# Kernel optimization log

Hardware: AMD Instinct MI355X
Metric: run time of the kernel (lower is better)

## Reference

```python
import jax, jax.numpy as jnp
import numpy as np

H, I, B, S = 3200, 12800, 8, 1024  # InternViT-6B MLP dims


def setup_inputs() -> dict:
    key = jax.random.key(0)
    ks = jax.random.split(key, 8)
    # int8-valued activations/weights stored as int32 (harness dtype set)
    hidden_states = jax.random.randint(ks[0], (B, S, H), -127, 128, dtype=jnp.int32)
    scale = jax.random.uniform(ks[1], (B * S,), dtype=jnp.float32) * 1e-3 + 1e-5
    w1 = jax.random.randint(ks[2], (I, H), -127, 128, dtype=jnp.int32)
    w1_scale = jax.random.uniform(ks[3], (I,), dtype=jnp.float32) * 1e-3 + 1e-5
    b1 = jax.random.normal(ks[4], (I,), dtype=jnp.float32) * 0.02
    w2 = jax.random.randint(ks[5], (H, I), -127, 128, dtype=jnp.int32)
    w2_scale = jax.random.uniform(ks[6], (H,), dtype=jnp.float32) * 1e-3 + 1e-5
    b2 = jax.random.normal(ks[7], (H,), dtype=jnp.float32) * 0.02
    return {"hidden_states": hidden_states, "scale": scale, "w1": w1,
            "w1_scale": w1_scale, "b1": b1, "w2": w2, "w2_scale": w2_scale, "b2": b2}


def _w8a8_linear(x_q, x_scale, w_q, w_scale, b):
    # enough that fp32 matmul reproduces the exact integer accumulator to
    # within float32 rounding of the final sum.
    acc = jnp.matmul(x_q.astype(jnp.float32), w_q.astype(jnp.float32).T)  # [T, out]
    out = acc * x_scale[:, None] * w_scale[None, :] + b[None, :]
    return out.astype(jnp.float16)


def reference(hidden_states, scale, w1, w1_scale, b1, w2, w2_scale, b2):
    bsz, seq, hidden = hidden_states.shape
    x_q = hidden_states.reshape(-1, hidden)                 # [T, H] int8 values
    # fc1: W8A8 -> fp16 with dynamic per-token input scale
    fc1_out = _w8a8_linear(x_q, scale, w1, w1_scale, b1)    # [T, I] fp16
    # fused gelu_and_quant: exact GELU, then per-token dynamic int8 re-quant
    g = jax.nn.gelu(fc1_out.astype(jnp.float32), approximate=False)  # [T, I]
    new_scale = jnp.max(jnp.abs(g), axis=-1) / 127.0        # dynamic per-token scale
    act_q = jnp.clip(jnp.round(g / new_scale[:, None]), -127, 127)  # int8 values
    # fc2: W8A8 -> fp16
    out = _w8a8_linear(act_q, new_scale, w2, w2_scale, b2)  # [T, H] fp16
    return out
```

## Files before the change

### kernel.cpp

```cpp
#include <hip/hip_runtime.h>
#include <hip/hip_bf16.h>
#include <hip/hip_fp16.h>

#define T_DIM 8192
#define H_DIM 3200
#define I_DIM 12800

typedef int v4i __attribute__((ext_vector_type(4)));
typedef _Float16 h8 __attribute__((ext_vector_type(8)));

__device__ __forceinline__ void gload16(const void* g, void* l) {
    __builtin_amdgcn_global_load_lds(
        (const __attribute__((address_space(1))) unsigned int*)g,
        (__attribute__((address_space(3))) unsigned int*)l, 16, 0, 0);
}

__global__ __launch_bounds__(256) void repack_kernel(const int* __restrict__ src,
                                                     unsigned int* __restrict__ dst,
                                                     long n4) {
    long i = (long)blockIdx.x * blockDim.x + threadIdx.x;
    long stride = (long)gridDim.x * blockDim.x;
    for (; i < n4; i += stride) {
        int4 v = ((const int4*)src)[i];
        dst[i] = (unsigned int)((v.x & 255) | ((v.y & 255) << 8) |
                                ((v.z & 255) << 16) | ((v.w & 255) << 24));
    }
}

template <int EPI>
__global__ __launch_bounds__(512, 2) void gemm_i8_8ph(
    const signed char* __restrict__ A, long strideA,
    const signed char* __restrict__ B, long strideB,
    int Ntrue, int K, int ldc,
    const float* __restrict__ rowscale, const float* __restrict__ colscale,
    const float* __restrict__ bias, void* __restrict__ Cout) {
    __shared__ signed char lds[131072];
    signed char* ldsA = lds;
    signed char* ldsB = lds + 65536;

    const int tid = threadIdx.x;
    const int lane = tid & 63, wid = tid >> 6;
    const int wr = wid >> 2, wc = wid & 3;
    const int bm = blockIdx.x, bn = blockIdx.y;
    const long Arow0 = (long)bm * 256;
    const long Bcol0 = (long)bn * 256;

    const int c0 = tid, c1 = tid + 512;
    const int r0 = c0 >> 2, r1 = c1 >> 2;
    const int s0 = (((c0 & 3) ^ ((r0 >> 1) & 3)) << 4);
    const int s1 = (((c1 & 3) ^ ((r1 >> 1) & 3)) << 4);
    const signed char* Ag0 = A + (Arow0 + r0) * strideA + s0;
    const signed char* Ag1 = A + (Arow0 + r1) * strideA + s1;
    const signed char* Bg0 = B + (Bcol0 + r0) * strideB + s0;
    const signed char* Bg1 = B + (Bcol0 + r1) * strideB + s1;
    const int d0 = c0 * 16, d1 = c1 * 16;

    const int NH = K >> 6;
    const int nkt = K >> 7;

#define STAGE_A(h)                                  \
    {                                               \
        const int hc_ = (h) < NH ? (h) : NH - 1;    \
        const long ko_ = (long)hc_ << 6;            \
        signed char* d_ = ldsA + (((h) & 3) << 14); \
        gload16(Ag0 + ko_, d_ + d0);                \
        gload16(Ag1 + ko_, d_ + d1);                \
    }
#define STAGE_B(h)                                  \
    {                                               \
        const int hc_ = (h) < NH ? (h) : NH - 1;    \
        const long ko_ = (long)hc_ << 6;            \
        signed char* d_ = ldsB + (((h) & 3) << 14); \
        gload16(Bg0 + ko_, d_ + d0);                \
        gload16(Bg1 + ko_, d_ + d1);                \
    }

    const int r = lane & 15, q = lane >> 4;
    const int swz = ((q ^ ((r >> 1) & 3)) << 4);
    const int aoff = (wr * 128 + r) * 64 + swz;
    const int boff = (wc * 64 + r) * 64 + swz;

    v4i acc[8][4] = {};
    v4i af[4], bf[4];

#define PHASE(SLOTA, SLOTB, AIDX, LOADB, ACCOFF, STAGE_STMT, GATE_STMT)     \
    {                                                                       \
        _Pragma("unroll") for (int i = 0; i < 4; ++i)                       \
            af[i] = *(const v4i*)((SLOTA) + aoff + ((AIDX) + i) * 1024);    \
        if (LOADB) {                                                        \
            _Pragma("unroll") for (int n = 0; n < 4; ++n)                   \
                bf[n] = *(const v4i*)((SLOTB) + boff + n * 1024);           \
        }                                                                   \
        STAGE_STMT;                                                         \
        __builtin_amdgcn_s_barrier();                                       \
        asm volatile("s_waitcnt lgkmcnt(0)");                               \
        __builtin_amdgcn_s_setprio(1);                                      \
        _Pragma("unroll") for (int m = 0; m < 4; ++m)                       \
            _Pragma("unroll") for (int n = 0; n < 4; ++n)                   \
                acc[m + (ACCOFF)][n] = __builtin_amdgcn_mfma_i32_16x16x64_i8( \
                    af[m], bf[n], acc[m + (ACCOFF)][n], 0, 0, 0);           \
        __builtin_amdgcn_s_setprio(0);                                      \
        GATE_STMT;                                                          \
        __builtin_amdgcn_s_barrier();                                       \
    }

    STAGE_B(0); STAGE_A(0); STAGE_B(1); STAGE_A(1);
    STAGE_B(2); STAGE_A(2); STAGE_B(3);
    asm volatile("s_waitcnt vmcnt(6)");
    __builtin_amdgcn_s_barrier();

    for (int kt = 0; kt < nkt; ++kt) {
        const int g = kt << 1;
        const signed char* sA0 = ldsA + ((g & 3) << 14);
        const signed char* sB0 = ldsB + ((g & 3) << 14);
        const signed char* sA1 = ldsA + (((g + 1) & 3) << 14);
        const signed char* sB1 = ldsB + (((g + 1) & 3) << 14);
        PHASE(sA0, sB0, 0, true, 0, STAGE_A(g + 3), );
        PHASE(sA0, sB0, 4, false, 4, STAGE_B(g + 4), );
        PHASE(sA1, sB1, 0, true, 0, STAGE_A(g + 4), );
        PHASE(sA1, sB1, 4, false, 4, STAGE_B(g + 5),
              asm volatile("s_waitcnt vmcnt(6)"));
    }

    const int row0 = bm * 256 + wr * 128;
    const int col0 = bn * 256 + wc * 64;
    const int r4 = (lane >> 4) << 2, cl = lane & 15;
#pragma unroll
    for (int m = 0; m < 8; ++m) {
        const int rowb = row0 + m * 16 + r4;
        float rs[4];
#pragma unroll
        for (int rr = 0; rr < 4; ++rr) rs[rr] = rowscale[rowb + rr];
#pragma unroll
        for (int n = 0; n < 4; ++n) {
            const int col = col0 + n * 16 + cl;
            if (col < Ntrue) {
                const float cs = colscale[col];
                const float bs = bias[col];
#pragma unroll
                for (int rr = 0; rr < 4; ++rr) {
                    float v = (float)acc[m][n][rr];
                    v = __fmul_rn(v, rs[rr]);
                    v = __fmul_rn(v, cs);
                    v = __fadd_rn(v, bs);
                    _Float16 hh = (_Float16)v;
                    const size_t idx = (size_t)(rowb + rr) * ldc + col;
                    if (EPI == 0) ((_Float16*)Cout)[idx] = hh;
                    else ((float*)Cout)[idx] = (float)hh;
                }
            }
        }
    }
#undef PHASE
#undef STAGE_A
#undef STAGE_B
}

__global__ __launch_bounds__(256) void gelu_quant(_Float16* __restrict__ fc1,
                                                  float* __restrict__ nscale) {
    __shared__ float gbuf[I_DIM];
    __shared__ float wmax[4];
    const int tid = threadIdx.x, lane = tid & 63, wid = tid >> 6;
    const long t = blockIdx.x;
    const h8* row = (const h8*)(fc1 + t * I_DIM);
    float lmax = 0.f;
    for (int c = tid; c < I_DIM / 8; c += 256) {
        h8 v = row[c];
#pragma unroll
        for (int j = 0; j < 8; ++j) {
            float x = (float)v[j];
            float e = erff(__fdiv_rn(x, 1.41421356237309504880f));
            float g = __fmul_rn(__fmul_rn(0.5f, x), __fadd_rn(1.0f, e));
            gbuf[c * 8 + j] = g;
            lmax = fmaxf(lmax, fabsf(g));
        }
    }
#pragma unroll
    for (int off = 32; off; off >>= 1) lmax = fmaxf(lmax, __shfl_xor(lmax, off, 64));
    if (lane == 0) wmax[wid] = lmax;
    __syncthreads();
    const float gmax = fmaxf(fmaxf(wmax[0], wmax[1]), fmaxf(wmax[2], wmax[3]));
    const float ns = gmax / 127.0f;
    if (tid == 0) nscale[t] = ns;
    unsigned long long* out = (unsigned long long*)(fc1 + t * I_DIM);
    for (int c = tid; c < I_DIM / 8; c += 256) {
        unsigned long long pk = 0;
#pragma unroll
        for (int j = 0; j < 8; ++j) {
            float qv = rintf(__fdiv_rn(gbuf[c * 8 + j], ns));
            qv = fminf(fmaxf(qv, -127.f), 127.f);
            pk |= ((unsigned long long)(unsigned char)(signed char)(int)qv) << (8 * j);
        }
        out[c] = pk;
    }
}

extern "C" void kernel_launch(void* const* d_in, const int* in_sizes, int n_in,
                              void* d_out, int out_size, void* d_ws, size_t ws_size,
                              hipStream_t stream) {
    const int* hs = (const int*)d_in[0];
    const float* scale = (const float*)d_in[1];
    const int* w1 = (const int*)d_in[2];
    const float* w1s = (const float*)d_in[3];
    const float* b1 = (const float*)d_in[4];
    const int* w2 = (const int*)d_in[5];
    const float* w2s = (const float*)d_in[6];
    const float* b2 = (const float*)d_in[7];

    char* ws = (char*)d_ws;
    signed char* xq = (signed char*)ws;
    signed char* w1q = xq + (size_t)T_DIM * H_DIM;
    signed char* w2q = w1q + (size_t)I_DIM * H_DIM;
    _Float16* fc1h = (_Float16*)(w2q + (size_t)H_DIM * I_DIM);
    const size_t fixed = (size_t)T_DIM * H_DIM + 2 * (size_t)I_DIM * H_DIM;

    int nc = 1;
    while (nc < 16) {
        size_t need = fixed + ((size_t)T_DIM / nc) * I_DIM * 2 +
                      ((size_t)T_DIM / nc) * 4 + 256;
        if (need <= ws_size) break;
        nc <<= 1;
    }
    const int chunkT = T_DIM / nc;
    float* nscale = (float*)((char*)fc1h + (size_t)chunkT * I_DIM * 2);

    repack_kernel<<<2048, 256, 0, stream>>>(hs, (unsigned int*)xq, (long)T_DIM * H_DIM / 4);
    repack_kernel<<<2048, 256, 0, stream>>>(w1, (unsigned int*)w1q, (long)I_DIM * H_DIM / 4);
    repack_kernel<<<2048, 256, 0, stream>>>(w2, (unsigned int*)w2q, (long)H_DIM * I_DIM / 4);

    const int n2tiles = (H_DIM + 255) / 256;
    for (int c = 0; c < nc; ++c) {
        const int t0 = c * chunkT;
        gemm_i8_8ph<0><<<dim3(chunkT / 256, I_DIM / 256), 512, 0, stream>>>(
            xq + (size_t)t0 * H_DIM, (long)H_DIM, w1q, (long)H_DIM,
            I_DIM, H_DIM, I_DIM,
            scale + t0, w1s, b1, (void*)fc1h);
        gelu_quant<<<chunkT, 256, 0, stream>>>(fc1h, nscale);
        gemm_i8_8ph<1><<<dim3(chunkT / 256, n2tiles), 512, 0, stream>>>(
            (const signed char*)fc1h, (long)I_DIM * 2, w2q, (long)I_DIM,
            H_DIM, I_DIM, H_DIM,
            nscale, w2s, b2,
            (void*)((float*)d_out + (size_t)t0 * H_DIM));
    }
}
```

Baseline: 966.1 us.

## Switch int8 GEMM to 32x32x32 MFMA with per-half-K pipeline and XCD remap

Rewrites the GEMM main loop to use 32x32x32 int8 MFMA instructions instead of 16x16x64, so each wave computes its 128x64 sub-tile with 8 larger accumulators. The loop is restructured to process one 64-wide K slice per iteration with a 3-deep LDS prefetch, in place of the previous 8-phase schedule. Workgroup IDs are remapped so consecutive tiles land on the same XCD for better L2 reuse. The larger MFMA lowers LDS fragment traffic per flop, at the cost of a simpler, less interleaved schedule and an epilogue with strided rowscale loads.

```diff
diff --git a/kernel.cpp b/kernel.cpp
--- a/kernel.cpp
+++ b/kernel.cpp
@@ -7,6 +7,7 @@
 #define I_DIM 12800
 
 typedef int v4i __attribute__((ext_vector_type(4)));
+typedef int v16i __attribute__((ext_vector_type(16)));
 typedef _Float16 h8 __attribute__((ext_vector_type(8)));
 
 __device__ __forceinline__ void gload16(const void* g, void* l) {
@@ -28,7 +29,7 @@
 }
 
 template <int EPI>
-__global__ __launch_bounds__(512, 2) void gemm_i8_8ph(
+__global__ __launch_bounds__(512, 2) void gemm_i8_32x32(
     const signed char* __restrict__ A, long strideA,
     const signed char* __restrict__ B, long strideB,
     int Ntrue, int K, int ldc,
@@ -38,25 +39,35 @@
     signed char* ldsA = lds;
     signed char* ldsB = lds + 65536;
 
+    int bm, bn;
+    {
+        const int nwgx = gridDim.x;
+        const int nwg = nwgx * gridDim.y;
+        int id = blockIdx.x + nwgx * blockIdx.y;
+        const int q = nwg >> 3, r = nwg & 7;
+        const int x = id & 7, o = id >> 3;
+        id = (x < r ? x * (q + 1) : r * (q + 1) + (x - r) * q) + o;
+        bm = id % nwgx;
+        bn = id / nwgx;
+    }
+
     const int tid = threadIdx.x;
     const int lane = tid & 63, wid = tid >> 6;
     const int wr = wid >> 2, wc = wid & 3;
-    const int bm = blockIdx.x, bn = blockIdx.y;
     const long Arow0 = (long)bm * 256;
     const long Bcol0 = (long)bn * 256;
 
     const int c0 = tid, c1 = tid + 512;
-    const int r0 = c0 >> 2, r1 = c1 >> 2;
+    const int r0 = c0 >> 2, r1_ = c1 >> 2;
     const int s0 = (((c0 & 3) ^ ((r0 >> 1) & 3)) << 4);
-    const int s1 = (((c1 & 3) ^ ((r1 >> 1) & 3)) << 4);
+    const int s1 = (((c1 & 3) ^ ((r1_ >> 1) & 3)) << 4);
     const signed char* Ag0 = A + (Arow0 + r0) * strideA + s0;
-    const signed char* Ag1 = A + (Arow0 + r1) * strideA + s1;
+    const signed char* Ag1 = A + (Arow0 + r1_) * strideA + s1;
     const signed char* Bg0 = B + (Bcol0 + r0) * strideB + s0;
-    const signed char* Bg1 = B + (Bcol0 + r1) * strideB + s1;
+    const signed char* Bg1 = B + (Bcol0 + r1_) * strideB + s1;
     const int d0 = c0 * 16, d1 = c1 * 16;
 
     const int NH = K >> 6;
-    const int nkt = K >> 7;
 
 #define STAGE_A(h)                                  \
     {                                               \
@@ -75,83 +86,82 @@
         gload16(Bg1 + ko_, d_ + d1);                \
     }
 
-    const int r = lane & 15, q = lane >> 4;
-    const int swz = ((q ^ ((r >> 1) & 3)) << 4);
-    const int aoff = (wr * 128 + r) * 64 + swz;
-    const int boff = (wc * 64 + r) * 64 + swz;
-
-    v4i acc[8][4] = {};
-    v4i af[4], bf[4];
-
-#define PHASE(SLOTA, SLOTB, AIDX, LOADB, ACCOFF, STAGE_STMT, GATE_STMT)     \
-    {                                                                       \
-        _Pragma("unroll") for (int i = 0; i < 4; ++i)                       \
-            af[i] = *(const v4i*)((SLOTA) + aoff + ((AIDX) + i) * 1024);    \
-        if (LOADB) {                                                        \
-            _Pragma("unroll") for (int n = 0; n < 4; ++n)                   \
-                bf[n] = *(const v4i*)((SLOTB) + boff + n * 1024);           \
-        }                                                                   \
-        STAGE_STMT;                                                         \
-        __builtin_amdgcn_s_barrier();                                       \
-        asm volatile("s_waitcnt lgkmcnt(0)");                               \
-        __builtin_amdgcn_s_setprio(1);                                      \
-        _Pragma("unroll") for (int m = 0; m < 4; ++m)                       \
-            _Pragma("unroll") for (int n = 0; n < 4; ++n)                   \
-                acc[m + (ACCOFF)][n] = __builtin_amdgcn_mfma_i32_16x16x64_i8( \
-                    af[m], bf[n], acc[m + (ACCOFF)][n], 0, 0, 0);           \
-        __builtin_amdgcn_s_setprio(0);                                      \
-        GATE_STMT;                                                          \
-        __builtin_amdgcn_s_barrier();                                       \
-    }
-
-    STAGE_B(0); STAGE_A(0); STAGE_B(1); STAGE_A(1);
-    STAGE_B(2); STAGE_A(2); STAGE_B(3);
-    asm volatile("s_waitcnt vmcnt(6)");
+    const int rl = lane & 31, qh = lane >> 5;
+    const int x0 = ((qh ^ ((rl >> 1) & 3)) << 4);
+    const int aoff = (wr * 128 + rl) * 64 + x0;
+    const int boff = (wc * 64 + rl) * 64 + x0;
+
+    v16i acc[4][2] = {};
+
+    STAGE_A(0); STAGE_B(0); STAGE_A(1); STAGE_B(1); STAGE_A(2); STAGE_B(2);
+    asm volatile("s_waitcnt vmcnt(8)");
     __builtin_amdgcn_s_barrier();
 
-    for (int kt = 0; kt < nkt; ++kt) {
-        const int g = kt << 1;
-        const signed char* sA0 = ldsA + ((g & 3) << 14);
-        const signed char* sB0 = ldsB + ((g & 3) << 14);
-        const signed char* sA1 = ldsA + (((g + 1) & 3) << 14);
-        const signed char* sB1 = ldsB + (((g + 1) & 3) << 14);
-        PHASE(sA0, sB0, 0, true, 0, STAGE_A(g + 3), );
-        PHASE(sA0, sB0, 4, false, 4, STAGE_B(g + 4), );
-        PHASE(sA1, sB1, 0, true, 0, STAGE_A(g + 4), );
-        PHASE(sA1, sB1, 4, false, 4, STAGE_B(g + 5),
-              asm volatile("s_waitcnt vmcnt(6)"));
+    for (int h = 0; h < NH; ++h) {
+        const signed char* sA = ldsA + ((h & 3) << 14);
+        const signed char* sB = ldsB + ((h & 3) << 14);
+        v4i a0[4], a1[4], b0[2], b1[2];
+#pragma unroll
+        for (int m = 0; m < 4; ++m) {
+            a0[m] = *(const v4i*)(sA + (aoff + m * 2048));
+            a1[m] = *(const v4i*)(sA + ((aoff ^ 32) + m * 2048));
+        }
+#pragma unroll
+        for (int n = 0; n < 2; ++n) {
+            b0[n] = *(const v4i*)(sB + (boff + n * 2048));
+            b1[n] = *(const v4i*)(sB + ((boff ^ 32) + n * 2048));
+        }
+        STAGE_A(h + 3);
+        STAGE_B(h + 3);
+        __builtin_amdgcn_s_barrier();
+        asm volatile("s_waitcnt lgkmcnt(0)");
+        __builtin_amdgcn_s_setprio(1);
+#pragma unroll
+        for (int m = 0; m < 4; ++m)
+#pragma unroll
+            for (int n = 0; n < 2; ++n)
+                acc[m][n] = __builtin_amdgcn_mfma_i32_32x32x32_i8(
+                    a0[m], b0[n], acc[m][n], 0, 0, 0);
+#pragma unroll
+        for (int m = 0; m < 4; ++m)
+#pragma unroll
+            for (int n = 0; n < 2; ++n)
+                acc[m][n] = __builtin_amdgcn_mfma_i32_32x32x32_i8(
+                    a1[m], b1[n], acc[m][n], 0, 0, 0);
+        __builtin_amdgcn_s_setprio(0);
+        asm volatile("s_waitcnt vmcnt(8)");
+        __builtin_amdgcn_s_barrier();
     }
 
     const int row0 = bm * 256 + wr * 128;
     const int col0 = bn * 256 + wc * 64;
-    const int r4 = (lane >> 4) << 2, cl = lane & 15;
-#pragma unroll
-    for (int m = 0; m < 8; ++m) {
-        const int rowb = row0 + m * 16 + r4;
-        float rs[4];
-#pragma unroll
-        for (int rr = 0; rr < 4; ++rr) rs[rr] = rowscale[rowb + rr];
-#pragma unroll
-        for (int n = 0; n < 4; ++n) {
-            const int col = col0 + n * 16 + cl;
+    const int rbase = 4 * qh;
+#pragma unroll
+    for (int m = 0; m < 4; ++m) {
+#pragma unroll
+        for (int n = 0; n < 2; ++n) {
+            const int col = col0 + n * 32 + rl;
             if (col < Ntrue) {
                 const float cs = colscale[col];
                 const float bs = bias[col];
 #pragma unroll
-                for (int rr = 0; rr < 4; ++rr) {
-                    float v = (float)acc[m][n][rr];
-                    v = __fmul_rn(v, rs[rr]);
-                    v = __fmul_rn(v, cs);
-                    v = __fadd_rn(v, bs);
-                    _Float16 hh = (_Float16)v;
-                    const size_t idx = (size_t)(rowb + rr) * ldc + col;
-                    if (EPI == 0) ((_Float16*)Cout)[idx] = hh;
-                    else ((float*)Cout)[idx] = (float)hh;
+                for (int g = 0; g < 4; ++g) {
+#pragma unroll
+                    for (int rr = 0; rr < 4; ++rr) {
+                        const int row = row0 + m * 32 + rbase + 8 * g + rr;
+                        float v = (float)acc[m][n][g * 4 + rr];
+                        v = __fmul_rn(v, rowscale[row]);
+                        v = __fmul_rn(v, cs);
+                        v = __fadd_rn(v, bs);
+                        _Float16 hh = (_Float16)v;
+                        const size_t idx = (size_t)row * ldc + col;
+                        if (EPI == 0) ((_Float16*)Cout)[idx] = hh;
+                        else ((float*)Cout)[idx] = (float)hh;
+                    }
                 }
             }
         }
     }
-#undef PHASE
 #undef STAGE_A
 #undef STAGE_B
 }
@@ -231,12 +241,12 @@
     const int n2tiles = (H_DIM + 255) / 256;
     for (int c = 0; c < nc; ++c) {
         const int t0 = c * chunkT;
-        gemm_i8_8ph<0><<<dim3(chunkT / 256, I_DIM / 256), 512, 0, stream>>>(
+        gemm_i8_32x32<0><<<dim3(chunkT / 256, I_DIM / 256), 512, 0, stream>>>(
             xq + (size_t)t0 * H_DIM, (long)H_DIM, w1q, (long)H_DIM,
             I_DIM, H_DIM, I_DIM,
             scale + t0, w1s, b1, (void*)fc1h);
         gelu_quant<<<chunkT, 256, 0, stream>>>(fc1h, nscale);
-        gemm_i8_8ph<1><<<dim3(chunkT / 256, n2tiles), 512, 0, stream>>>(
+        gemm_i8_32x32<1><<<dim3(chunkT / 256, n2tiles), 512, 0, stream>>>(
             (const signed char*)fc1h, (long)I_DIM * 2, w2q, (long)I_DIM,
             H_DIM, I_DIM, H_DIM,
             nscale, w2s, b2,
```

Result: slower. 1.078 ms (+11.6%).
